# Optimization experiments

Hardware: AMD Instinct MI355X
Metric: run time of the kernel (lower is better)

## Reference

```python
import jax, jax.numpy as jnp
import numpy as np

N_NODES = 50000
N_EDGES = 800000
D_IN = 128
D_OUT = 128
HEADS = 2
NEG_SLOPE = 0.2  # PyG GATConv default


def _gat_layer(x, src, dst, W, att_src, att_dst, bias):
    """One PyG-style GATConv with concat=False (mean over heads).
    x: [N, d_in], W: [d_in, H*d_out], att_src/att_dst: [H, d_out], bias: [d_out].
    Edge (j=src -> i=dst); softmax normalized over incoming edges of each dst node.
    """
    n = x.shape[0]
    d_out = att_src.shape[1]
    h = (x @ W).reshape(n, HEADS, d_out)                       # [N, H, D]
    a_s = jnp.einsum('nhd,hd->nh', h, att_src)                 # [N, H]
    a_d = jnp.einsum('nhd,hd->nh', h, att_dst)                 # [N, H]
    e = jax.nn.leaky_relu(a_s[src] + a_d[dst], NEG_SLOPE)      # [E, H]
    # numerically stable segment softmax over dst
    m = jax.ops.segment_max(e, dst, num_segments=n)            # [N, H]
    p = jnp.exp(e - m[dst])                                    # [E, H]
    s = jax.ops.segment_sum(p, dst, num_segments=n)            # [N, H]
    alpha = p / s[dst]                                         # [E, H]
    msg = h[src] * alpha[:, :, None]                           # [E, H, D]
    out = jax.ops.segment_sum(msg, dst, num_segments=n)        # [N, H, D]
    return out.mean(axis=1) + bias                             # concat=False -> mean heads


def setup_inputs() -> dict:
    key = jax.random.key(0)
    ks = jax.random.split(key, 10)
    sc = 0.05
    return {
        'x': jax.random.normal(ks[0], (N_NODES, D_IN), dtype=jnp.float32),
        'edge_index': jax.random.randint(ks[1], (2, N_EDGES), 0, N_NODES, dtype=jnp.int64),
        'W1': jax.random.normal(ks[2], (D_IN, HEADS * D_IN), dtype=jnp.float32) * sc,
        'att_src1': jax.random.normal(ks[3], (HEADS, D_IN), dtype=jnp.float32) * sc,
        'att_dst1': jax.random.normal(ks[4], (HEADS, D_IN), dtype=jnp.float32) * sc,
        'b1': jnp.zeros((D_IN,), dtype=jnp.float32),
        'W2': jax.random.normal(ks[5], (D_IN, HEADS * D_OUT), dtype=jnp.float32) * sc,
        'att_src2': jax.random.normal(ks[6], (HEADS, D_OUT), dtype=jnp.float32) * sc,
        'att_dst2': jax.random.normal(ks[7], (HEADS, D_OUT), dtype=jnp.float32) * sc,
        'b2': jnp.zeros((D_OUT,), dtype=jnp.float32),
    }


def reference(x, edge_index, W1, att_src1, att_dst1, b1, W2, att_src2, att_dst2, b2):
    n = x.shape[0]
    # PyG GATConv adds self-loops by default -> every node has >=1 incoming edge
    loops = jnp.arange(n, dtype=edge_index.dtype)
    src = jnp.concatenate([edge_index[0], loops])
    dst = jnp.concatenate([edge_index[1], loops])
    x = _gat_layer(x, src, dst, W1, att_src1, att_dst1, b1)
    x = _gat_layer(x, src, dst, W2, att_src2, att_dst2, b2)
    return x
```

## Files before the change

### kernel.cpp

```cpp
#include <hip/hip_runtime.h>
#include <hip/hip_bf16.h>

#define D 128
#define NCOLS 256
#define NPB 256
#define CAP 12288
#define P1CHUNK 4096

using f16x8 = __attribute__((ext_vector_type(8))) _Float16;
using f16x2 = __attribute__((ext_vector_type(2))) _Float16;
using f32x4 = __attribute__((ext_vector_type(4))) float;

__global__ void detect_kernel(const void* __restrict__ ei, int* __restrict__ flag,
                              int* __restrict__ gcnt) {
    gcnt[threadIdx.x] = 0;
    if (threadIdx.x == 0) *flag = 0;
    __syncthreads();
    const unsigned* u = (const unsigned*)ei;
    if (u[2 * threadIdx.x + 1] != 0) *flag = 1;
}

__device__ inline int edge_val(const void* ei, int is32, long long idx) {
    if (is32) return ((const int*)ei)[idx];
    return (int)(((const long long*)ei)[idx]);
}

__global__ __launch_bounds__(256) void bin_kernel(
    const void* __restrict__ ei, const int* __restrict__ flag,
    unsigned* __restrict__ bins, int* __restrict__ gcnt, int E, int nbuck) {
    __shared__ unsigned stage[P1CHUNK];
    __shared__ int cnt[256], offs[256], cur[256], gb[256];
    int tid = threadIdx.x;
    int base = blockIdx.x * P1CHUNK;
    int m = min(P1CHUNK, E - base);
    int is32 = *flag;
    cnt[tid] = 0; cur[tid] = 0;
    __syncthreads();
    unsigned pk[16]; int bb[16];
    int cn = 0;
    for (int i = tid; i < m; i += 256) {
        int src = edge_val(ei, is32, base + i);
        int dst = edge_val(ei, is32, (long long)E + base + i);
        int b = dst >> 8;
        pk[cn] = ((unsigned)b << 24) | ((unsigned)(dst & 255) << 16) | (unsigned)src;
        bb[cn] = b;
        ++cn;
        atomicAdd(&cnt[b], 1);
    }
    __syncthreads();
    offs[tid] = cnt[tid];
    __syncthreads();
#pragma unroll
    for (int off = 1; off < 256; off <<= 1) {
        int u = (tid >= off) ? offs[tid - off] : 0;
        __syncthreads();
        offs[tid] += u;
        __syncthreads();
    }
    if (tid < nbuck && cnt[tid] > 0) gb[tid] = atomicAdd(&gcnt[tid], cnt[tid]);
    else gb[tid] = 0;
    __syncthreads();
    for (int k = 0; k < cn; ++k) {
        int b = bb[k];
        int p = (offs[b] - cnt[b]) + atomicAdd(&cur[b], 1);
        stage[p] = pk[k];
    }
    __syncthreads();
    for (int i = tid; i < m; i += 256) {
        unsigned it = stage[i];
        int b = (int)(it >> 24);
        int local = i - (offs[b] - cnt[b]);
        int gpos = gb[b] + local;
        if (gpos < CAP) bins[(size_t)b * CAP + gpos] = it & 0x00FFFFFFu;
    }
}

__global__ void bscan_kernel(const int* __restrict__ gcnt, int* __restrict__ bbase,
                             int nbuck, int n) {
    __shared__ int a[256];
    int tid = threadIdx.x;
    int t = 0;
    if (tid < nbuck) {
        int lo = tid * NPB, hi = min(n, lo + NPB);
        t = min(gcnt[tid], CAP) + (hi - lo);
    }
    a[tid] = t;
    __syncthreads();
#pragma unroll
    for (int off = 1; off < 256; off <<= 1) {
        int u = (tid >= off) ? a[tid - off] : 0;
        __syncthreads();
        a[tid] += u;
        __syncthreads();
    }
    if (tid < nbuck) bbase[tid] = a[tid] - t;
}

__global__ __launch_bounds__(256) void build_kernel(
    const unsigned* __restrict__ bins, const int* __restrict__ gcnt,
    const int* __restrict__ bbase, int* __restrict__ row_ptr,
    int* __restrict__ csr_src, int n) {
    __shared__ unsigned items[CAP];
    __shared__ int deg[256], sc[256], cur[256];
    int b = blockIdx.x, tid = threadIdx.x;
    int node0 = b * NPB;
    int nn = min(n - node0, NPB);
    int cnt = min(gcnt[b], CAP);
    const unsigned* src = bins + (size_t)b * CAP;
    for (int i = tid; i < cnt; i += 256) items[i] = src[i];
    deg[tid] = (tid < nn) ? 1 : 0;
    __syncthreads();
    for (int i = tid; i < cnt; i += 256) atomicAdd(&deg[(items[i] >> 16) & 255], 1);
    __syncthreads();
    int d = deg[tid];
    sc[tid] = d;
    __syncthreads();
#pragma unroll
    for (int off = 1; off < 256; off <<= 1) {
        int u = (tid >= off) ? sc[tid - off] : 0;
        __syncthreads();
        sc[tid] += u;
        __syncthreads();
    }
    int incl = sc[tid];
    int excl = incl - d;
    int gb = bbase[b];
    if (tid < nn) row_ptr[node0 + tid + 1] = gb + incl;
    if (b == 0 && tid == 0) row_ptr[0] = 0;
    cur[tid] = excl + ((tid < nn) ? 1 : 0);
    if (tid < nn) csr_src[gb + excl] = node0 + tid;
    __syncthreads();
    for (int i = tid; i < cnt; i += 256) {
        unsigned it = items[i];
        int p = atomicAdd(&cur[(it >> 16) & 255], 1);
        csr_src[gb + p] = (int)(it & 0xFFFFu);
    }
}

__global__ __launch_bounds__(256) void attprep_kernel(
    const float* __restrict__ W1, const float* __restrict__ as1,
    const float* __restrict__ ad1, float* __restrict__ v_s1,
    float* __restrict__ v_d1, _Float16* __restrict__ wT1,
    const float* __restrict__ W2, const float* __restrict__ as2,
    const float* __restrict__ ad2, float* __restrict__ v_s2,
    float* __restrict__ v_d2, _Float16* __restrict__ wT2) {
    int layer = blockIdx.x >= 17;
    int bx = blockIdx.x - (layer ? 17 : 0);
    const float* W = layer ? W2 : W1;
    const float* att_s = layer ? as2 : as1;
    const float* att_d = layer ? ad2 : ad1;
    float* v_s = layer ? v_s2 : v_s1;
    float* v_d = layer ? v_d2 : v_d1;
    _Float16* wT = layer ? wT2 : wT1;
    int tid = threadIdx.x;
    if (bx == 16) {
        int h = tid >> 7, d = tid & 127;
        const float* wrow = W + d * NCOLS + h * D;
        const float* as = att_s + h * D;
        const float* ad = att_d + h * D;
        float ss = 0.f, sd = 0.f;
        for (int i = 0; i < D; i += 4) {
            float4 wv = *reinterpret_cast<const float4*>(wrow + i);
            float4 av = *reinterpret_cast<const float4*>(as + i);
            float4 dv = *reinterpret_cast<const float4*>(ad + i);
            ss += wv.x * av.x + wv.y * av.y + wv.z * av.z + wv.w * av.w;
            sd += wv.x * dv.x + wv.y * dv.y + wv.z * dv.z + wv.w * dv.w;
        }
        v_s[tid] = ss;
        v_d[tid] = sd;
    } else {
        int base = bx * 2048 + tid * 8;
#pragma unroll
        for (int t = 0; t < 8; t += 4) {
            int f = base + t;
            int kk = f >> 7, i = f & 127;
            int h = kk >> 7, d = kk & 127;
            float4 wv = *reinterpret_cast<const float4*>(W + d * NCOLS + h * D + i);
            wT[(size_t)(i + 0) * NCOLS + kk] = (_Float16)(0.5f * wv.x);
            wT[(size_t)(i + 1) * NCOLS + kk] = (_Float16)(0.5f * wv.y);
            wT[(size_t)(i + 2) * NCOLS + kk] = (_Float16)(0.5f * wv.z);
            wT[(size_t)(i + 3) * NCOLS + kk] = (_Float16)(0.5f * wv.w);
        }
    }
}

__global__ __launch_bounds__(256) void prep_x_kernel(
    const float* __restrict__ x, const float* __restrict__ v_s,
    const float* __restrict__ v_d, _Float16* __restrict__ xh,
    float* __restrict__ a_s, float* __restrict__ a_d, int n) {
    int lane = threadIdx.x & 63;
    int node = blockIdx.x * 4 + (threadIdx.x >> 6);
    if (node >= n) return;
    float2 xv = *reinterpret_cast<const float2*>(x + (size_t)node * D + 2 * lane);
    f16x2 hx = {(_Float16)xv.x, (_Float16)xv.y};
    *reinterpret_cast<f16x2*>(xh + (size_t)node * D + 2 * lane) = hx;
    float2 vs0 = *reinterpret_cast<const float2*>(v_s + 2 * lane);
    float2 vs1 = *reinterpret_cast<const float2*>(v_s + D + 2 * lane);
    float2 vd0 = *reinterpret_cast<const float2*>(v_d + 2 * lane);
    float2 vd1 = *reinterpret_cast<const float2*>(v_d + D + 2 * lane);
    float s0 = xv.x * vs0.x + xv.y * vs0.y;
    float s1 = xv.x * vs1.x + xv.y * vs1.y;
    float d0 = xv.x * vd0.x + xv.y * vd0.y;
    float d1 = xv.x * vd1.x + xv.y * vd1.y;
#pragma unroll
    for (int off = 1; off < 64; off <<= 1) {
        s0 += __shfl_xor(s0, off, 64);
        s1 += __shfl_xor(s1, off, 64);
        d0 += __shfl_xor(d0, off, 64);
        d1 += __shfl_xor(d1, off, 64);
    }
    if (lane == 0) {
        *reinterpret_cast<float2*>(a_s + (size_t)node * 2) = make_float2(s0, s1);
        *reinterpret_cast<float2*>(a_d + (size_t)node * 2) = make_float2(d0, d1);
    }
}

__global__ __launch_bounds__(256) void aggregate_kernel(
    const _Float16* __restrict__ xh, const float* __restrict__ a_s,
    const float* __restrict__ a_d, const int* __restrict__ row_ptr,
    const int* __restrict__ csr_src, _Float16* __restrict__ aggh, int n) {
    int lane = threadIdx.x & 63;
    int node = blockIdx.x * 4 + (threadIdx.x >> 6);
    if (node >= n) return;
    int beg = row_ptr[node], end = row_ptr[node + 1];
    float2 ad = *reinterpret_cast<const float2*>(a_d + (size_t)node * 2);
    int sub = lane >> 4, cq = lane & 15;
    float s0 = 0.f, s1 = 0.f;
    float acc0[8] = {}, acc1[8] = {};
    const _Float16* xb = xh + 8 * cq;
    for (int chunk = beg; chunk < end; chunk += 64) {
        int cnt = min(64, end - chunk);
        int j_l = 0;
        unsigned pp_l = 0;
        if (lane < cnt) {
            j_l = csr_src[chunk + lane];
            float2 as2 = *reinterpret_cast<const float2*>(a_s + (size_t)j_l * 2);
            float e0 = as2.x + ad.x; e0 = (e0 > 0.f) ? e0 : 0.2f * e0;
            float e1 = as2.y + ad.y; e1 = (e1 > 0.f) ? e1 : 0.2f * e1;
            f16x2 pq = {(_Float16)__expf(e0), (_Float16)__expf(e1)};
            pp_l = __builtin_bit_cast(unsigned, pq);
            s0 += (float)pq[0];
            s1 += (float)pq[1];
        }
#pragma unroll 4
        for (int k = 0; k < cnt; k += 4) {
            int idx = k + sub;
            unsigned ppu = (unsigned)__shfl((int)pp_l, idx, 64);
            int j = __shfl(j_l, idx, 64);
            f16x2 pq = __builtin_bit_cast(f16x2, ppu);
            float p0 = (float)pq[0], p1 = (float)pq[1];
            f16x8 hv = *reinterpret_cast<const f16x8*>(xb + (size_t)j * D);
#pragma unroll
            for (int i = 0; i < 8; ++i) {
                float h = (float)hv[i];
                acc0[i] += p0 * h;
                acc1[i] += p1 * h;
            }
        }
    }
#pragma unroll
    for (int i = 0; i < 8; ++i) {
        acc0[i] += __shfl_xor(acc0[i], 16, 64);
        acc0[i] += __shfl_xor(acc0[i], 32, 64);
        acc1[i] += __shfl_xor(acc1[i], 16, 64);
        acc1[i] += __shfl_xor(acc1[i], 32, 64);
    }
#pragma unroll
    for (int off = 1; off < 64; off <<= 1) {
        s0 += __shfl_xor(s0, off, 64);
        s1 += __shfl_xor(s1, off, 64);
    }
    if (sub == 0) {
        float i0 = 1.f / s0, i1 = 1.f / s1;
        f16x8 o0, o1;
#pragma unroll
        for (int i = 0; i < 8; ++i) {
            o0[i] = (_Float16)(acc0[i] * i0);
            o1[i] = (_Float16)(acc1[i] * i1);
        }
        *reinterpret_cast<f16x8*>(aggh + (size_t)node * NCOLS + 8 * cq)     = o0;
        *reinterpret_cast<f16x8*>(aggh + (size_t)node * NCOLS + D + 8 * cq) = o1;
    }
}

__global__ __launch_bounds__(256) void mfma_out_kernel(
    const _Float16* __restrict__ aggh, const _Float16* __restrict__ wT,
    const float* __restrict__ bias, const float* __restrict__ vs_next,
    const float* __restrict__ vd_next, float* __restrict__ as_next,
    float* __restrict__ ad_next, float* __restrict__ outf,
    _Float16* __restrict__ outh, int n) {
    int tid = threadIdx.x;
    int wave = tid >> 6, lane = tid & 63;
    int m0 = blockIdx.x * 64 + wave * 16;
    int ml = lane & 15;
    int g  = lane >> 4;
    int arow = m0 + ml; if (arow >= n) arow = n - 1;
    const _Float16* aA = aggh + (size_t)arow * NCOLS + 8 * g;
    const _Float16* bB = wT + (size_t)ml * NCOLS + 8 * g;

    f32x4 acc[8] = {};
#pragma unroll
    for (int kt = 0; kt < 8; ++kt) {
        int ko = kt * 32;
        f16x8 av = *reinterpret_cast<const f16x8*>(aA + ko);
#pragma unroll
        for (int nt = 0; nt < 8; ++nt) {
            f16x8 bv = *reinterpret_cast<const f16x8*>(bB + nt * 16 * NCOLS + ko);
            acc[nt] = __builtin_amdgcn_mfma_f32_16x16x32_f16(av, bv, acc[nt], 0, 0, 0);
        }
    }

    float bv8[8], vs0v[8], vs1v[8], vd0v[8], vd1v[8];
#pragma unroll
    for (int nt = 0; nt < 8; ++nt) bv8[nt] = bias[nt * 16 + ml];
    if (vs_next) {
#pragma unroll
        for (int nt = 0; nt < 8; ++nt) {
            int col = nt * 16 + ml;
            vs0v[nt] = vs_next[col];
            vs1v[nt] = vs_next[D + col];
            vd0v[nt] = vd_next[col];
            vd1v[nt] = vd_next[D + col];
        }
    }

#pragma unroll
    for (int r = 0; r < 4; ++r) {
        int orow = m0 + g * 4 + r;
        float vrow[8];
#pragma unroll
        for (int nt = 0; nt < 8; ++nt) vrow[nt] = acc[nt][r] + bv8[nt];
        if (orow < n) {
            if (outf) {
#pragma unroll
                for (int nt = 0; nt < 8; ++nt)
                    outf[(size_t)orow * D + nt * 16 + ml] = vrow[nt];
            }
            if (outh) {
#pragma unroll
                for (int nt = 0; nt < 8; ++nt)
                    outh[(size_t)orow * D + nt * 16 + ml] = (_Float16)vrow[nt];
            }
        }
        if (vs_next) {
            float ps0 = 0.f, ps1 = 0.f, pd0 = 0.f, pd1 = 0.f;
#pragma unroll
            for (int nt = 0; nt < 8; ++nt) {
                ps0 += vrow[nt] * vs0v[nt];
                ps1 += vrow[nt] * vs1v[nt];
                pd0 += vrow[nt] * vd0v[nt];
                pd1 += vrow[nt] * vd1v[nt];
            }
#pragma unroll
            for (int off = 1; off < 16; off <<= 1) {
                ps0 += __shfl_xor(ps0, off, 64);
                ps1 += __shfl_xor(ps1, off, 64);
                pd0 += __shfl_xor(pd0, off, 64);
                pd1 += __shfl_xor(pd1, off, 64);
            }
            if (ml == 0 && orow < n) {
                *reinterpret_cast<float2*>(as_next + (size_t)orow * 2) = make_float2(ps0, ps1);
                *reinterpret_cast<float2*>(ad_next + (size_t)orow * 2) = make_float2(pd0, pd1);
            }
        }
    }
}

extern "C" void kernel_launch(void* const* d_in, const int* in_sizes, int n_in,
                              void* d_out, int out_size, void* d_ws, size_t ws_size,
                              hipStream_t stream) {
    const float* x    = (const float*)d_in[0];
    const void*  ei   = d_in[1];
    const float* W1   = (const float*)d_in[2];
    const float* as1v = (const float*)d_in[3];
    const float* ad1v = (const float*)d_in[4];
    const float* b1   = (const float*)d_in[5];
    const float* W2   = (const float*)d_in[6];
    const float* as2v = (const float*)d_in[7];
    const float* ad2v = (const float*)d_in[8];
    const float* b2   = (const float*)d_in[9];
    float* out = (float*)d_out;

    const int N  = in_sizes[0] / D;
    const int E  = in_sizes[1] / 2;
    const int ET = E + N;
    const int NBUCK = (N + NPB - 1) / NPB;

    char* w = (char*)d_ws;
    size_t off = 0;
    auto alloc = [&](size_t bytes) {
        void* p = w + off;
        off = (off + bytes + 15) & ~(size_t)15;
        return p;
    };
    int*      flag    = (int*)     alloc(16);
    int*      gcnt    = (int*)     alloc(256 * 4);
    int*      bbase   = (int*)     alloc(256 * 4);
    unsigned* bins    = (unsigned*)alloc((size_t)NBUCK * CAP * 4);
    int*      row_ptr = (int*)     alloc((size_t)(N + 1) * 4);
    int*      csr_src = (int*)     alloc((size_t)ET * 4);
    float*    v_s1    = (float*)   alloc(NCOLS * 4);
    float*    v_d1    = (float*)   alloc(NCOLS * 4);
    _Float16* wT1     = (_Float16*)alloc((size_t)NCOLS * D * 2);
    float*    v_s2    = (float*)   alloc(NCOLS * 4);
    float*    v_d2    = (float*)   alloc(NCOLS * 4);
    _Float16* wT2     = (_Float16*)alloc((size_t)NCOLS * D * 2);
    float*    a_s1    = (float*)   alloc((size_t)N * 2 * 4);
    float*    a_d1    = (float*)   alloc((size_t)N * 2 * 4);
    float*    a_s2    = (float*)   alloc((size_t)N * 2 * 4);
    float*    a_d2    = (float*)   alloc((size_t)N * 2 * 4);
    _Float16* xh      = (_Float16*)alloc((size_t)N * D * 2);
    _Float16* xmh     = (_Float16*)alloc((size_t)N * D * 2);
    _Float16* aggh    = (_Float16*)alloc((size_t)N * NCOLS * 2);

    hipLaunchKernelGGL(detect_kernel, dim3(1), dim3(256), 0, stream, ei, flag, gcnt);
    hipLaunchKernelGGL(bin_kernel, dim3((E + P1CHUNK - 1) / P1CHUNK), dim3(256), 0, stream,
                       ei, flag, bins, gcnt, E, NBUCK);
    hipLaunchKernelGGL(bscan_kernel, dim3(1), dim3(256), 0, stream, gcnt, bbase, NBUCK, N);
    hipLaunchKernelGGL(build_kernel, dim3(NBUCK), dim3(256), 0, stream,
                       bins, gcnt, bbase, row_ptr, csr_src, N);

    hipLaunchKernelGGL(attprep_kernel, dim3(34), dim3(256), 0, stream,
                       W1, as1v, ad1v, v_s1, v_d1, wT1,
                       W2, as2v, ad2v, v_s2, v_d2, wT2);

    hipLaunchKernelGGL(prep_x_kernel, dim3((N + 3) / 4), dim3(256), 0, stream,
                       x, v_s1, v_d1, xh, a_s1, a_d1, N);
    hipLaunchKernelGGL(aggregate_kernel, dim3((N + 3) / 4), dim3(256), 0, stream,
                       xh, a_s1, a_d1, row_ptr, csr_src, aggh, N);
    hipLaunchKernelGGL(mfma_out_kernel, dim3((N + 63) / 64), dim3(256), 0, stream,
                       aggh, wT1, b1, v_s2, v_d2, a_s2, a_d2,
                       (float*)nullptr, xmh, N);

    hipLaunchKernelGGL(aggregate_kernel, dim3((N + 3) / 4), dim3(256), 0, stream,
                       xmh, a_s2, a_d2, row_ptr, csr_src, aggh, N);
    hipLaunchKernelGGL(mfma_out_kernel, dim3((N + 63) / 64), dim3(256), 0, stream,
                       aggh, wT2, b2, (const float*)nullptr, (const float*)nullptr,
                       (float*)nullptr, (float*)nullptr, out, (_Float16*)nullptr, N);
}
```

Measured before the change: 221.8 us.

## Fold detect and bucket scan into neighbouring kernels, simplify binning

The detect_kernel work moves into an extra block of attprep_kernel, and the bscan_kernel is removed: each build block now computes its own global base with a reduction over earlier buckets' counts. bin_kernel drops the shared-memory staging and scan. It counts per bucket first, then re-reads the edges and scatters directly to global bins using local atomics. This removes two launches and one shared-memory pass, at the cost of reading the edge list twice in bin_kernel and writing to global memory less coalesced.

```diff
diff --git a/kernel.cpp b/kernel.cpp
--- a/kernel.cpp
+++ b/kernel.cpp
@@ -11,130 +11,9 @@
 using f16x2 = __attribute__((ext_vector_type(2))) _Float16;
 using f32x4 = __attribute__((ext_vector_type(4))) float;
 
-__global__ void detect_kernel(const void* __restrict__ ei, int* __restrict__ flag,
-                              int* __restrict__ gcnt) {
-    gcnt[threadIdx.x] = 0;
-    if (threadIdx.x == 0) *flag = 0;
-    __syncthreads();
-    const unsigned* u = (const unsigned*)ei;
-    if (u[2 * threadIdx.x + 1] != 0) *flag = 1;
-}
-
 __device__ inline int edge_val(const void* ei, int is32, long long idx) {
     if (is32) return ((const int*)ei)[idx];
     return (int)(((const long long*)ei)[idx]);
-}
-
-__global__ __launch_bounds__(256) void bin_kernel(
-    const void* __restrict__ ei, const int* __restrict__ flag,
-    unsigned* __restrict__ bins, int* __restrict__ gcnt, int E, int nbuck) {
-    __shared__ unsigned stage[P1CHUNK];
-    __shared__ int cnt[256], offs[256], cur[256], gb[256];
-    int tid = threadIdx.x;
-    int base = blockIdx.x * P1CHUNK;
-    int m = min(P1CHUNK, E - base);
-    int is32 = *flag;
-    cnt[tid] = 0; cur[tid] = 0;
-    __syncthreads();
-    unsigned pk[16]; int bb[16];
-    int cn = 0;
-    for (int i = tid; i < m; i += 256) {
-        int src = edge_val(ei, is32, base + i);
-        int dst = edge_val(ei, is32, (long long)E + base + i);
-        int b = dst >> 8;
-        pk[cn] = ((unsigned)b << 24) | ((unsigned)(dst & 255) << 16) | (unsigned)src;
-        bb[cn] = b;
-        ++cn;
-        atomicAdd(&cnt[b], 1);
-    }
-    __syncthreads();
-    offs[tid] = cnt[tid];
-    __syncthreads();
-#pragma unroll
-    for (int off = 1; off < 256; off <<= 1) {
-        int u = (tid >= off) ? offs[tid - off] : 0;
-        __syncthreads();
-        offs[tid] += u;
-        __syncthreads();
-    }
-    if (tid < nbuck && cnt[tid] > 0) gb[tid] = atomicAdd(&gcnt[tid], cnt[tid]);
-    else gb[tid] = 0;
-    __syncthreads();
-    for (int k = 0; k < cn; ++k) {
-        int b = bb[k];
-        int p = (offs[b] - cnt[b]) + atomicAdd(&cur[b], 1);
-        stage[p] = pk[k];
-    }
-    __syncthreads();
-    for (int i = tid; i < m; i += 256) {
-        unsigned it = stage[i];
-        int b = (int)(it >> 24);
-        int local = i - (offs[b] - cnt[b]);
-        int gpos = gb[b] + local;
-        if (gpos < CAP) bins[(size_t)b * CAP + gpos] = it & 0x00FFFFFFu;
-    }
-}
-
-__global__ void bscan_kernel(const int* __restrict__ gcnt, int* __restrict__ bbase,
-                             int nbuck, int n) {
-    __shared__ int a[256];
-    int tid = threadIdx.x;
-    int t = 0;
-    if (tid < nbuck) {
-        int lo = tid * NPB, hi = min(n, lo + NPB);
-        t = min(gcnt[tid], CAP) + (hi - lo);
-    }
-    a[tid] = t;
-    __syncthreads();
-#pragma unroll
-    for (int off = 1; off < 256; off <<= 1) {
-        int u = (tid >= off) ? a[tid - off] : 0;
-        __syncthreads();
-        a[tid] += u;
-        __syncthreads();
-    }
-    if (tid < nbuck) bbase[tid] = a[tid] - t;
-}
-
-__global__ __launch_bounds__(256) void build_kernel(
-    const unsigned* __restrict__ bins, const int* __restrict__ gcnt,
-    const int* __restrict__ bbase, int* __restrict__ row_ptr,
-    int* __restrict__ csr_src, int n) {
-    __shared__ unsigned items[CAP];
-    __shared__ int deg[256], sc[256], cur[256];
-    int b = blockIdx.x, tid = threadIdx.x;
-    int node0 = b * NPB;
-    int nn = min(n - node0, NPB);
-    int cnt = min(gcnt[b], CAP);
-    const unsigned* src = bins + (size_t)b * CAP;
-    for (int i = tid; i < cnt; i += 256) items[i] = src[i];
-    deg[tid] = (tid < nn) ? 1 : 0;
-    __syncthreads();
-    for (int i = tid; i < cnt; i += 256) atomicAdd(&deg[(items[i] >> 16) & 255], 1);
-    __syncthreads();
-    int d = deg[tid];
-    sc[tid] = d;
-    __syncthreads();
-#pragma unroll
-    for (int off = 1; off < 256; off <<= 1) {
-        int u = (tid >= off) ? sc[tid - off] : 0;
-        __syncthreads();
-        sc[tid] += u;
-        __syncthreads();
-    }
-    int incl = sc[tid];
-    int excl = incl - d;
-    int gb = bbase[b];
-    if (tid < nn) row_ptr[node0 + tid + 1] = gb + incl;
-    if (b == 0 && tid == 0) row_ptr[0] = 0;
-    cur[tid] = excl + ((tid < nn) ? 1 : 0);
-    if (tid < nn) csr_src[gb + excl] = node0 + tid;
-    __syncthreads();
-    for (int i = tid; i < cnt; i += 256) {
-        unsigned it = items[i];
-        int p = atomicAdd(&cur[(it >> 16) & 255], 1);
-        csr_src[gb + p] = (int)(it & 0xFFFFu);
-    }
 }
 
 __global__ __launch_bounds__(256) void attprep_kernel(
@@ -143,7 +22,17 @@
     float* __restrict__ v_d1, _Float16* __restrict__ wT1,
     const float* __restrict__ W2, const float* __restrict__ as2,
     const float* __restrict__ ad2, float* __restrict__ v_s2,
-    float* __restrict__ v_d2, _Float16* __restrict__ wT2) {
+    float* __restrict__ v_d2, _Float16* __restrict__ wT2,
+    const void* __restrict__ ei, int* __restrict__ flag, int* __restrict__ gcnt) {
+    int tid = threadIdx.x;
+    if (blockIdx.x == 34) {
+        gcnt[tid] = 0;
+        if (tid == 0) *flag = 0;
+        __syncthreads();
+        const unsigned* u = (const unsigned*)ei;
+        if (u[2 * tid + 1] != 0) *flag = 1;
+        return;
+    }
     int layer = blockIdx.x >= 17;
     int bx = blockIdx.x - (layer ? 17 : 0);
     const float* W = layer ? W2 : W1;
@@ -152,7 +41,6 @@
     float* v_s = layer ? v_s2 : v_s1;
     float* v_d = layer ? v_d2 : v_d1;
     _Float16* wT = layer ? wT2 : wT1;
-    int tid = threadIdx.x;
     if (bx == 16) {
         int h = tid >> 7, d = tid & 127;
         const float* wrow = W + d * NCOLS + h * D;
@@ -181,6 +69,85 @@
             wT[(size_t)(i + 2) * NCOLS + kk] = (_Float16)(0.5f * wv.z);
             wT[(size_t)(i + 3) * NCOLS + kk] = (_Float16)(0.5f * wv.w);
         }
+    }
+}
+
+__global__ __launch_bounds__(256) void bin_kernel(
+    const void* __restrict__ ei, const int* __restrict__ flag,
+    unsigned* __restrict__ bins, int* __restrict__ gcnt, int E, int nbuck) {
+    __shared__ int cnt[256], cur[256], gb[256];
+    int tid = threadIdx.x;
+    int base = blockIdx.x * P1CHUNK;
+    int m = min(P1CHUNK, E - base);
+    int is32 = *flag;
+    cnt[tid] = 0; cur[tid] = 0;
+    __syncthreads();
+    for (int i = tid; i < m; i += 256) {
+        int dst = edge_val(ei, is32, (long long)E + base + i);
+        atomicAdd(&cnt[dst >> 8], 1);
+    }
+    __syncthreads();
+    if (tid < nbuck && cnt[tid] > 0) gb[tid] = atomicAdd(&gcnt[tid], cnt[tid]);
+    else gb[tid] = 0;
+    __syncthreads();
+    for (int i = tid; i < m; i += 256) {
+        int src = edge_val(ei, is32, base + i);
+        int dst = edge_val(ei, is32, (long long)E + base + i);
+        int b = dst >> 8;
+        int pos = gb[b] + atomicAdd(&cur[b], 1);
+        if (pos < CAP)
+            bins[(size_t)b * CAP + pos] = ((unsigned)(dst & 255) << 16) | (unsigned)src;
+    }
+}
+
+__global__ __launch_bounds__(256) void build_kernel(
+    const unsigned* __restrict__ bins, const int* __restrict__ gcnt,
+    int* __restrict__ row_ptr, int* __restrict__ csr_src, int n, int nbuck) {
+    __shared__ unsigned items[CAP];
+    __shared__ int deg[256], sc[256], cur[256], pref[256];
+    int b = blockIdx.x, tid = threadIdx.x;
+    int node0 = b * NPB;
+    int nn = min(n - node0, NPB);
+    int cnt = min(gcnt[b], CAP);
+    int t = 0;
+    if (tid < b) {
+        int lo = tid * NPB, hi = min(n, lo + NPB);
+        t = min(gcnt[tid], CAP) + (hi - lo);
+    }
+    pref[tid] = t;
+    const unsigned* src = bins + (size_t)b * CAP;
+    for (int i = tid; i < cnt; i += 256) items[i] = src[i];
+    deg[tid] = (tid < nn) ? 1 : 0;
+    __syncthreads();
+#pragma unroll
+    for (int off = 128; off >= 1; off >>= 1) {
+        if (tid < off) pref[tid] += pref[tid + off];
+        __syncthreads();
+    }
+    int gb = pref[0];
+    for (int i = tid; i < cnt; i += 256) atomicAdd(&deg[(items[i] >> 16) & 255], 1);
+    __syncthreads();
+    int d = deg[tid];
+    sc[tid] = d;
+    __syncthreads();
+#pragma unroll
+    for (int off = 1; off < 256; off <<= 1) {
+        int u = (tid >= off) ? sc[tid - off] : 0;
+        __syncthreads();
+        sc[tid] += u;
+        __syncthreads();
+    }
+    int incl = sc[tid];
+    int excl = incl - d;
+    if (tid < nn) row_ptr[node0 + tid + 1] = gb + incl;
+    if (b == 0 && tid == 0) row_ptr[0] = 0;
+    cur[tid] = excl + ((tid < nn) ? 1 : 0);
+    if (tid < nn) csr_src[gb + excl] = node0 + tid;
+    __syncthreads();
+    for (int i = tid; i < cnt; i += 256) {
+        unsigned it = items[i];
+        int p = atomicAdd(&cur[(it >> 16) & 255], 1);
+        csr_src[gb + p] = (int)(it & 0xFFFFu);
     }
 }
 
@@ -395,7 +362,6 @@
     };
     int*      flag    = (int*)     alloc(16);
     int*      gcnt    = (int*)     alloc(256 * 4);
-    int*      bbase   = (int*)     alloc(256 * 4);
     unsigned* bins    = (unsigned*)alloc((size_t)NBUCK * CAP * 4);
     int*      row_ptr = (int*)     alloc((size_t)(N + 1) * 4);
     int*      csr_src = (int*)     alloc((size_t)ET * 4);
@@ -413,16 +379,13 @@
     _Float16* xmh     = (_Float16*)alloc((size_t)N * D * 2);
     _Float16* aggh    = (_Float16*)alloc((size_t)N * NCOLS * 2);
 
-    hipLaunchKernelGGL(detect_kernel, dim3(1), dim3(256), 0, stream, ei, flag, gcnt);
+    hipLaunchKernelGGL(attprep_kernel, dim3(35), dim3(256), 0, stream,
+                       W1, as1v, ad1v, v_s1, v_d1, wT1,
+                       W2, as2v, ad2v, v_s2, v_d2, wT2, ei, flag, gcnt);
     hipLaunchKernelGGL(bin_kernel, dim3((E + P1CHUNK - 1) / P1CHUNK), dim3(256), 0, stream,
                        ei, flag, bins, gcnt, E, NBUCK);
-    hipLaunchKernelGGL(bscan_kernel, dim3(1), dim3(256), 0, stream, gcnt, bbase, NBUCK, N);
     hipLaunchKernelGGL(build_kernel, dim3(NBUCK), dim3(256), 0, stream,
-                       bins, gcnt, bbase, row_ptr, csr_src, N);
-
-    hipLaunchKernelGGL(attprep_kernel, dim3(34), dim3(256), 0, stream,
-                       W1, as1v, ad1v, v_s1, v_d1, wT1,
-                       W2, as2v, ad2v, v_s2, v_d2, wT2);
+                       bins, gcnt, row_ptr, csr_src, N, NBUCK);
 
     hipLaunchKernelGGL(prep_x_kernel, dim3((N + 3) / 4), dim3(256), 0, stream,
                        x, v_s1, v_d1, xh, a_s1, a_d1, N);
```

After: 217.4 us. 1.02x faster.
